# Optimization experiments

Measured on AMD Instinct MI355X. Metric: run time of the kernel, lower is better.

## Reference

```python
import jax, jax.numpy as jnp
import numpy as np

N_NODES = 50000
N_EDGES = 800000
F_IN = 128
F_OUT = 128
N_REL = 4
BN_EPS = 1e-5


def setup_inputs() -> dict:
    key = jax.random.key(0)
    ks = jax.random.split(key, 12)
    s = 1.0 / np.sqrt(F_IN)
    inp = {
        "x": jax.random.normal(ks[0], (N_NODES, F_IN), dtype=jnp.float32),
        "edge_index": jax.random.randint(ks[1], (2, N_EDGES), 0, N_NODES, dtype=jnp.int64),
        "edge_type": jax.random.randint(ks[2], (N_EDGES,), 0, N_REL, dtype=jnp.int64),
        # self-loop linear
        "W_self": jax.random.uniform(ks[3], (F_IN, F_OUT), jnp.float32, -s, s),
        "b_self": jax.random.uniform(ks[4], (F_OUT,), jnp.float32, -s, s),
        # per-relation GIN MLP: Linear -> BatchNorm1d -> ReLU -> Linear (stacked over relations)
        "W1": jax.random.uniform(ks[5], (N_REL, F_IN, F_OUT), jnp.float32, -s, s),
        "b1": jax.random.uniform(ks[6], (N_REL, F_OUT), jnp.float32, -s, s),
        "gamma": jnp.ones((N_REL, F_OUT), jnp.float32),
        "beta": jnp.zeros((N_REL, F_OUT), jnp.float32),
        "W2": jax.random.uniform(ks[7], (N_REL, F_OUT, F_OUT), jnp.float32, -1.0 / np.sqrt(F_OUT), 1.0 / np.sqrt(F_OUT)),
        "b2": jax.random.uniform(ks[8], (N_REL, F_OUT), jnp.float32, -1.0 / np.sqrt(F_OUT), 1.0 / np.sqrt(F_OUT)),
    }
    return inp


def reference(x, edge_index, edge_type, W_self, b_self, W1, b1, gamma, beta, W2, b2):
    N = x.shape[0]
    R = W1.shape[0]
    src, dst = edge_index[0], edge_index[1]
    # single fused scatter-add over (relation, dst): segment id = rel*N + dst
    msg = x[src]                                        # [E, F_in]
    seg = edge_type * N + dst                           # [E]
    agg = jax.ops.segment_sum(msg, seg, num_segments=R * N).reshape(R, N, -1)  # [R, N, F_in]
    # GIN with eps=0: h = x + sum of neighbor messages, per relation
    h = x[None, :, :] + agg                             # [R, N, F_in]
    # MLP: Linear -> BatchNorm1d (batch stats over nodes) -> ReLU -> Linear
    h = jnp.einsum('rnf,rfg->rng', h, W1) + b1[:, None, :]
    mean = jnp.mean(h, axis=1, keepdims=True)
    var = jnp.var(h, axis=1, keepdims=True)
    h = (h - mean) * jax.lax.rsqrt(var + BN_EPS) * gamma[:, None, :] + beta[:, None, :]
    h = jax.nn.relu(h)
    out_rel = jnp.einsum('rng,rgk->rnk', h, W2) + b2[:, None, :]  # [R, N, F_out]
    return x @ W_self + b_self + jnp.sum(out_rel, axis=0)
```

## Files before the change

### kernel.cpp

```cpp
#include <hip/hip_runtime.h>

#define NN 50000
#define NE 800000
#define F 128
#define NREL 4
#define RN (NREL * NN)
#define NB 196
#define BN_EPS 1e-5f
#define TILE 128
#define NT1 391
#define LDW 136
#define CTS 132

typedef __attribute__((ext_vector_type(8))) short short8;
typedef __attribute__((ext_vector_type(4))) float floatx4;

__device__ __forceinline__ ushort f2bf(float f) {
    union { float f; unsigned u; } v; v.f = f;
    unsigned r = v.u + 0x7fffu + ((v.u >> 16) & 1u);
    return (ushort)(r >> 16);
}
__device__ __forceinline__ float bf2f(ushort h) {
    union { unsigned u; float f; } v; v.u = ((unsigned)h) << 16;
    return v.f;
}
__device__ __forceinline__ float ubf(unsigned bits) {
    union { unsigned u; float f; } v; v.u = bits; return v.f;
}
__device__ __forceinline__ unsigned pk2(float a, float b) {
    return (unsigned)f2bf(a) | ((unsigned)f2bf(b) << 16);
}
__device__ __forceinline__ void acc_u4(float* acc, uint4 v) {
    acc[0] += ubf(v.x << 16); acc[1] += ubf(v.x & 0xffff0000u);
    acc[2] += ubf(v.y << 16); acc[3] += ubf(v.y & 0xffff0000u);
    acc[4] += ubf(v.z << 16); acc[5] += ubf(v.z & 0xffff0000u);
    acc[6] += ubf(v.w << 16); acc[7] += ubf(v.w & 0xffff0000u);
}

__global__ __launch_bounds__(256) void xb_kernel(
    const float* __restrict__ x, ushort* __restrict__ xb)
{
    int i = blockIdx.x * 256 + threadIdx.x;
    float4 v = *(const float4*)(x + (size_t)i * 4);
    uint2 u;
    u.x = pk2(v.x, v.y);
    u.y = pk2(v.z, v.w);
    *(uint2*)(xb + (size_t)i * 4) = u;
}

__global__ __launch_bounds__(256) void hist_kernel(
    const int* __restrict__ ei, const int* __restrict__ et, int* __restrict__ counts)
{
    int e = blockIdx.x * 256 + threadIdx.x;
    if (e >= NE) return;
    atomicAdd(&counts[et[e] * NN + ei[NE + e]], 1);
}

__global__ __launch_bounds__(256) void scan1_kernel(
    const int* __restrict__ counts, int* __restrict__ rowptr, int* __restrict__ bsum)
{
    __shared__ int wsum[4];
    const int tid = threadIdx.x;
    const int base = blockIdx.x * 1024 + tid * 4;
    int c[4];
    #pragma unroll
    for (int j = 0; j < 4; j++) c[j] = (base + j < RN) ? counts[base + j] : 0;
    int tsum = c[0] + c[1] + c[2] + c[3];
    const int lane = tid & 63, wv = tid >> 6;
    int s = tsum;
    #pragma unroll
    for (int d = 1; d < 64; d <<= 1) { int t = __shfl_up(s, d); if (lane >= d) s += t; }
    if (lane == 63) wsum[wv] = s;
    __syncthreads();
    int wave_off = 0;
    #pragma unroll
    for (int w = 0; w < 4; w++) if (w < wv) wave_off += wsum[w];
    int run = wave_off + s - tsum;
    #pragma unroll
    for (int j = 0; j < 4; j++) {
        if (base + j < RN) rowptr[base + j] = run;
        run += c[j];
    }
    if (tid == 0) bsum[blockIdx.x] = wsum[0] + wsum[1] + wsum[2] + wsum[3];
}

__global__ __launch_bounds__(256) void scan2_kernel(
    const int* __restrict__ bsum, int* __restrict__ boff, int* __restrict__ rowptr)
{
    __shared__ int wsum[4];
    const int tid = threadIdx.x;
    int v = (tid < NB) ? bsum[tid] : 0;
    const int lane = tid & 63, wv = tid >> 6;
    int s = v;
    #pragma unroll
    for (int d = 1; d < 64; d <<= 1) { int t = __shfl_up(s, d); if (lane >= d) s += t; }
    if (lane == 63) wsum[wv] = s;
    __syncthreads();
    int wave_off = 0;
    #pragma unroll
    for (int w = 0; w < 4; w++) if (w < wv) wave_off += wsum[w];
    if (tid < NB) boff[tid] = wave_off + s - v;
    if (tid == 0) rowptr[RN] = wsum[0] + wsum[1] + wsum[2] + wsum[3];
}

__global__ __launch_bounds__(256) void scan3_kernel(
    int* __restrict__ rowptr, const int* __restrict__ boff, int* __restrict__ cursor)
{
    const int base = blockIdx.x * 1024 + threadIdx.x * 4;
    const int off = boff[blockIdx.x];
    #pragma unroll
    for (int j = 0; j < 4; j++) {
        int idx = base + j;
        if (idx < RN) { int v = rowptr[idx] + off; rowptr[idx] = v; cursor[idx] = v; }
    }
}

__global__ __launch_bounds__(256) void reorder_kernel(
    const int* __restrict__ ei, const int* __restrict__ et,
    int* __restrict__ cursor, int* __restrict__ sorted_src)
{
    int e = blockIdx.x * 256 + threadIdx.x;
    if (e >= NE) return;
    int key = et[e] * NN + ei[NE + e];
    int pos = atomicAdd(&cursor[key], 1);
    sorted_src[pos] = ei[e];
}

__global__ __launch_bounds__(256) void gather_kernel(
    const ushort* __restrict__ xb, const int* __restrict__ rowptr,
    const int* __restrict__ sorted_src, ushort* __restrict__ hbuf)
{
    const int t = blockIdx.x * 256 + threadIdx.x;
    const int row = t >> 4;
    const int lane = t & 15;
    const int n = row % NN;

    const uint4* xv = (const uint4*)xb;
    float acc[8];
    {
        uint4 v = xv[n * 16 + lane];
        acc[0] = ubf(v.x << 16); acc[1] = ubf(v.x & 0xffff0000u);
        acc[2] = ubf(v.y << 16); acc[3] = ubf(v.y & 0xffff0000u);
        acc[4] = ubf(v.z << 16); acc[5] = ubf(v.z & 0xffff0000u);
        acc[6] = ubf(v.w << 16); acc[7] = ubf(v.w & 0xffff0000u);
    }
    int e = rowptr[row];
    const int e1 = rowptr[row + 1];
    for (; e + 4 <= e1; e += 4) {
        int s0 = sorted_src[e], s1 = sorted_src[e + 1];
        int s2 = sorted_src[e + 2], s3 = sorted_src[e + 3];
        uint4 a = xv[s0 * 16 + lane];
        uint4 b = xv[s1 * 16 + lane];
        uint4 c = xv[s2 * 16 + lane];
        uint4 d = xv[s3 * 16 + lane];
        acc_u4(acc, a); acc_u4(acc, b); acc_u4(acc, c); acc_u4(acc, d);
    }
    for (; e < e1; ++e) {
        int s0 = sorted_src[e];
        acc_u4(acc, xv[s0 * 16 + lane]);
    }
    uint4 o;
    o.x = pk2(acc[0], acc[1]);
    o.y = pk2(acc[2], acc[3]);
    o.z = pk2(acc[4], acc[5]);
    o.w = pk2(acc[6], acc[7]);
    *(uint4*)(hbuf + (size_t)row * F + lane * 8) = o;
}

__global__ __launch_bounds__(256) void prep_kernel(
    const float* __restrict__ W1, const float* __restrict__ W2,
    const float* __restrict__ Wself, ushort* __restrict__ Wt_g)
{
    __shared__ ushort Lt[F * F];
    int m = blockIdx.x;
    const float* src = (m < 4) ? (W1 + (size_t)m * F * F)
                     : (m < 8) ? (W2 + (size_t)(m - 4) * F * F)
                               : Wself;
    int tid = threadIdx.x;
    #pragma unroll
    for (int p = 0; p < 16; p++) {
        int i4 = tid + p * 256;
        int k = i4 >> 5;
        int n4 = (i4 & 31) * 4;
        float4 v = *(const float4*)(src + (size_t)k * F + n4);
        Lt[(n4 + 0) * F + k] = f2bf(v.x);
        Lt[(n4 + 1) * F + k] = f2bf(v.y);
        Lt[(n4 + 2) * F + k] = f2bf(v.z);
        Lt[(n4 + 3) * F + k] = f2bf(v.w);
    }
    __syncthreads();
    #pragma unroll
    for (int p = 0; p < 8; p++) {
        int c = tid + p * 256;
        *(uint4*)(Wt_g + (size_t)m * F * F + c * 8) = *(const uint4*)&Lt[c * 8];
    }
}

__global__ __launch_bounds__(256, 4) void gemm1_kernel(
    ushort* __restrict__ hbuf, const ushort* __restrict__ Wt_g,
    const float* __restrict__ b1, float* __restrict__ partials)
{
    __shared__ __attribute__((aligned(16))) ushort Wt[F * LDW];
    __shared__ float csum[F], csq[F];

    const int tid = threadIdx.x;
    const int r = blockIdx.y;
    const int n0 = blockIdx.x * TILE;
    const int lane = tid & 63, w = tid >> 6;
    const int m = lane & 15, quad = lane >> 4;

    if (tid < F) { csum[tid] = 0.f; csq[tid] = 0.f; }

    {
        const ushort* wg = Wt_g + (size_t)r * F * F;
        #pragma unroll
        for (int p = 0; p < 8; p++) {
            int c = tid + p * 256;
            int n = c >> 4, off = (c & 15) * 8;
            *(uint4*)&Wt[n * LDW + off] = *(const uint4*)(wg + c * 8);
        }
    }
    __syncthreads();

    const ushort* Ap0 = hbuf + ((size_t)r * NN + n0 + w * 32 + m) * F + quad * 8;
    const ushort* Ap1 = Ap0 + 16 * F;
    const ushort* Bp  = &Wt[m * LDW + quad * 8];

    floatx4 acc[2][8];
    #pragma unroll
    for (int rg = 0; rg < 2; rg++)
        #pragma unroll
        for (int g = 0; g < 8; g++) acc[rg][g] = (floatx4)0.f;

    #pragma unroll
    for (int kk = 0; kk < 4; kk++) {
        short8 a0 = *(const short8*)(Ap0 + kk * 32);
        short8 a1 = *(const short8*)(Ap1 + kk * 32);
        #pragma unroll
        for (int g = 0; g < 8; g++) {
            short8 b = *(const short8*)(Bp + g * 16 * LDW + kk * 32);
            acc[0][g] = __builtin_amdgcn_mfma_f32_16x16x32_bf16(a0, b, acc[0][g], 0, 0, 0);
            acc[1][g] = __builtin_amdgcn_mfma_f32_16x16x32_bf16(a1, b, acc[1][g], 0, 0, 0);
        }
    }
    __syncthreads();

    ushort* At = Wt;
    #pragma unroll
    for (int rg = 0; rg < 2; rg++) {
        const int rb = w * 32 + rg * 16;
        #pragma unroll
        for (int g = 0; g < 8; g++) {
            int c = g * 16 + m;
            float bv = b1[r * F + c];
            float ls = 0.f, lq = 0.f;
            #pragma unroll
            for (int i = 0; i < 4; i++) {
                int lrow = rb + quad * 4 + i;
                float v = acc[rg][g][i] + bv;
                At[lrow * LDW + c] = f2bf(v);
                if (n0 + lrow < NN) { ls += v; lq += v * v; }
            }
            ls += __shfl_xor(ls, 16); ls += __shfl_xor(ls, 32);
            lq += __shfl_xor(lq, 16); lq += __shfl_xor(lq, 32);
            if (quad == 0) { atomicAdd(&csum[c], ls); atomicAdd(&csq[c], lq); }
        }
    }
    __syncthreads();

    #pragma unroll
    for (int p = 0; p < 8; p++) {
        int cc = tid + p * 256;
        int row = cc >> 4, off = (cc & 15) * 8;
        if (n0 + row < NN)
            *(uint4*)(hbuf + ((size_t)r * NN + n0 + row) * F + off) =
                *(const uint4*)&At[row * LDW + off];
    }
    partials[((size_t)r * NT1 + blockIdx.x) * 256 + tid] =
        (tid < F) ? csum[tid] : csq[tid - F];
}

__global__ __launch_bounds__(256) void bncoef_kernel(
    const float* __restrict__ partials,
    const float* __restrict__ gamma, const float* __restrict__ beta,
    const float* __restrict__ b2, const float* __restrict__ bself,
    float* __restrict__ sa, float* __restrict__ sb, float* __restrict__ btot)
{
    const int tid = threadIdx.x;
    const int pair = blockIdx.x * 8 + (tid >> 5);
    const int l32 = tid & 31;
    const int rel = pair >> 7, col = pair & 127;
    const float* p = partials + (size_t)rel * NT1 * 256;
    float s = 0.f, q = 0.f;
    for (int b = l32; b < NT1; b += 32) {
        s += p[b * 256 + col];
        q += p[b * 256 + 128 + col];
    }
    #pragma unroll
    for (int d = 1; d < 32; d <<= 1) {
        s += __shfl_xor(s, d, 32);
        q += __shfl_xor(q, d, 32);
    }
    if (l32 == 0) {
        float mean = s * (1.0f / NN);
        float var = q * (1.0f / NN) - mean * mean;
        float g = gamma[pair] * rsqrtf(var + BN_EPS);
        sa[pair] = g;
        sb[pair] = beta[pair] - mean * g;
    }
    if (blockIdx.x == 0 && tid < F)
        btot[tid] = bself[tid] + b2[tid] + b2[F + tid] + b2[2 * F + tid] + b2[3 * F + tid];
}

__global__ __launch_bounds__(256, 4) void gemm2_kernel(
    const ushort* __restrict__ xb, const ushort* __restrict__ h1,
    const ushort* __restrict__ Wt_g,
    const float* __restrict__ sa, const float* __restrict__ sb,
    const float* __restrict__ btot, float* __restrict__ out)
{
    __shared__ __attribute__((aligned(16))) ushort Wt[F * LDW];
    __shared__ float sAl[NREL * F], sBl[NREL * F];

    const int tid = threadIdx.x;
    const int n0 = blockIdx.x * TILE;
    const int lane = tid & 63, w = tid >> 6;
    const int m = lane & 15, quad = lane >> 4;
    const int koff = quad * 8;

    #pragma unroll
    for (int p = 0; p < 2; p++) {
        int idx = tid + p * 256;
        sAl[idx] = sa[idx];
        sBl[idx] = sb[idx];
    }

    floatx4 acc[2][8];
    #pragma unroll
    for (int rg = 0; rg < 2; rg++)
        #pragma unroll
        for (int g = 0; g < 8; g++) acc[rg][g] = (floatx4)0.f;

    for (int rel = 0; rel < 5; rel++) {
        __syncthreads();
        {
            int mat = (rel < 4) ? (NREL + rel) : 8;
            const ushort* wg = Wt_g + (size_t)mat * F * F;
            #pragma unroll
            for (int p = 0; p < 8; p++) {
                int c = tid + p * 256;
                int n = c >> 4, off = (c & 15) * 8;
                *(uint4*)&Wt[n * LDW + off] = *(const uint4*)(wg + c * 8);
            }
        }
        __syncthreads();
        const ushort* Bp = &Wt[m * LDW + koff];
        if (rel < 4) {
            const ushort* hp0 = h1 + ((size_t)rel * NN + n0 + w * 32 + m) * F + koff;
            const ushort* hp1 = hp0 + 16 * F;
            #pragma unroll
            for (int kk = 0; kk < 4; kk++) {
                uint4 rv0 = *(const uint4*)(hp0 + kk * 32);
                uint4 rv1 = *(const uint4*)(hp1 + kk * 32);
                float4 ca0 = *(const float4*)(&sAl[rel * F + koff + kk * 32]);
                float4 ca1 = *(const float4*)(&sAl[rel * F + koff + kk * 32 + 4]);
                float4 cb0 = *(const float4*)(&sBl[rel * F + koff + kk * 32]);
                float4 cb1 = *(const float4*)(&sBl[rel * F + koff + kk * 32 + 4]);
                union { uint4 u; short8 s; } a0, a1;
                a0.u.x = pk2(fmaxf(fmaf(ubf(rv0.x << 16),         ca0.x, cb0.x), 0.f),
                             fmaxf(fmaf(ubf(rv0.x & 0xffff0000u), ca0.y, cb0.y), 0.f));
                a0.u.y = pk2(fmaxf(fmaf(ubf(rv0.y << 16),         ca0.z, cb0.z), 0.f),
                             fmaxf(fmaf(ubf(rv0.y & 0xffff0000u), ca0.w, cb0.w), 0.f));
                a0.u.z = pk2(fmaxf(fmaf(ubf(rv0.z << 16),         ca1.x, cb1.x), 0.f),
                             fmaxf(fmaf(ubf(rv0.z & 0xffff0000u), ca1.y, cb1.y), 0.f));
                a0.u.w = pk2(fmaxf(fmaf(ubf(rv0.w << 16),         ca1.z, cb1.z), 0.f),
                             fmaxf(fmaf(ubf(rv0.w & 0xffff0000u), ca1.w, cb1.w), 0.f));
                a1.u.x = pk2(fmaxf(fmaf(ubf(rv1.x << 16),         ca0.x, cb0.x), 0.f),
                             fmaxf(fmaf(ubf(rv1.x & 0xffff0000u), ca0.y, cb0.y), 0.f));
                a1.u.y = pk2(fmaxf(fmaf(ubf(rv1.y << 16),         ca0.z, cb0.z), 0.f),
                             fmaxf(fmaf(ubf(rv1.y & 0xffff0000u), ca0.w, cb0.w), 0.f));
                a1.u.z = pk2(fmaxf(fmaf(ubf(rv1.z << 16),         ca1.x, cb1.x), 0.f),
                             fmaxf(fmaf(ubf(rv1.z & 0xffff0000u), ca1.y, cb1.y), 0.f));
                a1.u.w = pk2(fmaxf(fmaf(ubf(rv1.w << 16),         ca1.z, cb1.z), 0.f),
                             fmaxf(fmaf(ubf(rv1.w & 0xffff0000u), ca1.w, cb1.w), 0.f));
                #pragma unroll
                for (int g = 0; g < 8; g++) {
                    short8 b = *(const short8*)(Bp + g * 16 * LDW + kk * 32);
                    acc[0][g] = __builtin_amdgcn_mfma_f32_16x16x32_bf16(a0.s, b, acc[0][g], 0, 0, 0);
                    acc[1][g] = __builtin_amdgcn_mfma_f32_16x16x32_bf16(a1.s, b, acc[1][g], 0, 0, 0);
                }
            }
        } else {
            const ushort* xp0 = xb + (size_t)(n0 + w * 32 + m) * F + koff;
            const ushort* xp1 = xp0 + 16 * F;
            #pragma unroll
            for (int kk = 0; kk < 4; kk++) {
                short8 a0 = *(const short8*)(xp0 + kk * 32);
                short8 a1 = *(const short8*)(xp1 + kk * 32);
                #pragma unroll
                for (int g = 0; g < 8; g++) {
                    short8 b = *(const short8*)(Bp + g * 16 * LDW + kk * 32);
                    acc[0][g] = __builtin_amdgcn_mfma_f32_16x16x32_bf16(a0, b, acc[0][g], 0, 0, 0);
                    acc[1][g] = __builtin_amdgcn_mfma_f32_16x16x32_bf16(a1, b, acc[1][g], 0, 0, 0);
                }
            }
        }
    }

    float* Ct = (float*)Wt;
    #pragma unroll
    for (int half = 0; half < 2; half++) {
        __syncthreads();
        if ((w >> 1) == half) {
            const int wl = w & 1;
            #pragma unroll
            for (int rg = 0; rg < 2; rg++) {
                const int rb = wl * 32 + rg * 16;
                #pragma unroll
                for (int g = 0; g < 8; g++) {
                    int c = g * 16 + m;
                    float bv = btot[c];
                    #pragma unroll
                    for (int i = 0; i < 4; i++) {
                        int lrow = rb + quad * 4 + i;
                        Ct[lrow * CTS + c] = acc[rg][g][i] + bv;
                    }
                }
            }
        }
        __syncthreads();
        #pragma unroll
        for (int p = 0; p < 8; p++) {
            int i4 = tid + p * 256;
            int row = i4 >> 5;
            int c4 = (i4 & 31) * 4;
            int n = n0 + half * 64 + row;
            if (n < NN)
                *(float4*)(out + (size_t)n * F + c4) = *(const float4*)&Ct[row * CTS + c4];
        }
    }
}

extern "C" void kernel_launch(void* const* d_in, const int* in_sizes, int n_in,
                              void* d_out, int out_size, void* d_ws, size_t ws_size,
                              hipStream_t stream) {
    const float* x     = (const float*)d_in[0];
    const int*   ei    = (const int*)d_in[1];
    const int*   et    = (const int*)d_in[2];
    const float* Wself = (const float*)d_in[3];
    const float* bself = (const float*)d_in[4];
    const float* W1    = (const float*)d_in[5];
    const float* b1    = (const float*)d_in[6];
    const float* gamma = (const float*)d_in[7];
    const float* beta  = (const float*)d_in[8];
    const float* W2    = (const float*)d_in[9];
    const float* b2    = (const float*)d_in[10];
    float* out = (float*)d_out;

    ushort* hbuf = (ushort*)d_ws;
    ushort* xb   = hbuf + (size_t)RN * F;
    ushort* Wt_g = xb + (size_t)NN * F;
    float*  partials = (float*)(Wt_g + 9 * F * F);
    float*  sa    = partials + (size_t)NREL * NT1 * 256;
    float*  sb    = sa + NREL * F;
    float*  btot  = sb + NREL * F;
    int* counts     = (int*)(btot + F);
    int* rowptr     = counts + RN;
    int* cursor     = rowptr + RN + 1;
    int* sorted_src = cursor + RN;
    int* bsum       = sorted_src + NE;
    int* boff       = bsum + 256;

    hipMemsetAsync(counts, 0, (size_t)RN * sizeof(int), stream);

    prep_kernel<<<9, 256, 0, stream>>>(W1, W2, Wself, Wt_g);
    xb_kernel<<<NN * F / 1024, 256, 0, stream>>>(x, xb);
    hist_kernel<<<(NE + 255) / 256, 256, 0, stream>>>(ei, et, counts);
    scan1_kernel<<<NB, 256, 0, stream>>>(counts, rowptr, bsum);
    scan2_kernel<<<1, 256, 0, stream>>>(bsum, boff, rowptr);
    scan3_kernel<<<NB, 256, 0, stream>>>(rowptr, boff, cursor);
    reorder_kernel<<<(NE + 255) / 256, 256, 0, stream>>>(ei, et, cursor, sorted_src);
    gather_kernel<<<RN * 16 / 256, 256, 0, stream>>>(xb, rowptr, sorted_src, hbuf);
    {
        dim3 grid(NT1, NREL);
        gemm1_kernel<<<grid, 256, 0, stream>>>(hbuf, Wt_g, b1, partials);
    }
    bncoef_kernel<<<64, 256, 0, stream>>>(partials, gamma, beta, b2, bself, sa, sb, btot);
    gemm2_kernel<<<NT1, 256, 0, stream>>>(xb, hbuf, Wt_g, sa, sb, btot, out);
}
```

Baseline: 344.9 us.

## Merge prep kernels, fold scan2 into scan3, widen gemm2 to 512 threads

Merges the bf16 conversion of x, the weight transpose and the edge histogram into one launch. It also folds the single-block block-sum scan into scan3, where every block rescans the 196 partial sums itself. Together these remove three kernel launches and their dependency gaps. gemm2 now uses 512 threads with 16 rows per wave, so each wave holds half the accumulators, in exchange for less A-operand reuse per wave. The merged prep kernel reserves 32KB of LDS for every block, which may lower occupancy for the xb and histogram blocks.

```diff
diff --git a/kernel.cpp b/kernel.cpp
--- a/kernel.cpp
+++ b/kernel.cpp
@@ -11,6 +11,8 @@
 #define NT1 391
 #define LDW 136
 #define CTS 132
+#define XBB 6250
+#define HISTB 3125
 
 typedef __attribute__((ext_vector_type(8))) short short8;
 typedef __attribute__((ext_vector_type(4))) float floatx4;
@@ -19,10 +21,6 @@
     union { float f; unsigned u; } v; v.f = f;
     unsigned r = v.u + 0x7fffu + ((v.u >> 16) & 1u);
     return (ushort)(r >> 16);
-}
-__device__ __forceinline__ float bf2f(ushort h) {
-    union { unsigned u; float f; } v; v.u = ((unsigned)h) << 16;
-    return v.f;
 }
 __device__ __forceinline__ float ubf(unsigned bits) {
     union { unsigned u; float f; } v; v.u = bits; return v.f;
@@ -37,23 +35,48 @@
     acc[6] += ubf(v.w << 16); acc[7] += ubf(v.w & 0xffff0000u);
 }
 
-__global__ __launch_bounds__(256) void xb_kernel(
-    const float* __restrict__ x, ushort* __restrict__ xb)
-{
-    int i = blockIdx.x * 256 + threadIdx.x;
-    float4 v = *(const float4*)(x + (size_t)i * 4);
-    uint2 u;
-    u.x = pk2(v.x, v.y);
-    u.y = pk2(v.z, v.w);
-    *(uint2*)(xb + (size_t)i * 4) = u;
-}
-
-__global__ __launch_bounds__(256) void hist_kernel(
+__global__ __launch_bounds__(256) void prep_all_kernel(
+    const float* __restrict__ x, ushort* __restrict__ xb,
+    const float* __restrict__ W1, const float* __restrict__ W2,
+    const float* __restrict__ Wself, ushort* __restrict__ Wt_g,
     const int* __restrict__ ei, const int* __restrict__ et, int* __restrict__ counts)
 {
-    int e = blockIdx.x * 256 + threadIdx.x;
-    if (e >= NE) return;
-    atomicAdd(&counts[et[e] * NN + ei[NE + e]], 1);
+    __shared__ ushort Lt[F * F];
+    const int tid = threadIdx.x;
+    const int b = blockIdx.x;
+    if (b < XBB) {
+        int i = b * 256 + tid;
+        float4 v = *(const float4*)(x + (size_t)i * 4);
+        uint2 u;
+        u.x = pk2(v.x, v.y);
+        u.y = pk2(v.z, v.w);
+        *(uint2*)(xb + (size_t)i * 4) = u;
+    } else if (b < XBB + 9) {
+        int m = b - XBB;
+        const float* src = (m < 4) ? (W1 + (size_t)m * F * F)
+                         : (m < 8) ? (W2 + (size_t)(m - 4) * F * F)
+                                   : Wself;
+        #pragma unroll
+        for (int p = 0; p < 16; p++) {
+            int i4 = tid + p * 256;
+            int k = i4 >> 5;
+            int n4 = (i4 & 31) * 4;
+            float4 v = *(const float4*)(src + (size_t)k * F + n4);
+            Lt[(n4 + 0) * F + k] = f2bf(v.x);
+            Lt[(n4 + 1) * F + k] = f2bf(v.y);
+            Lt[(n4 + 2) * F + k] = f2bf(v.z);
+            Lt[(n4 + 3) * F + k] = f2bf(v.w);
+        }
+        __syncthreads();
+        #pragma unroll
+        for (int p = 0; p < 8; p++) {
+            int c = tid + p * 256;
+            *(uint4*)(Wt_g + (size_t)m * F * F + c * 8) = *(const uint4*)&Lt[c * 8];
+        }
+    } else {
+        int e = (b - XBB - 9) * 256 + tid;
+        if (e < NE) atomicAdd(&counts[et[e] * NN + ei[NE + e]], 1);
+    }
 }
 
 __global__ __launch_bounds__(256) void scan1_kernel(
@@ -84,10 +107,11 @@
     if (tid == 0) bsum[blockIdx.x] = wsum[0] + wsum[1] + wsum[2] + wsum[3];
 }
 
-__global__ __launch_bounds__(256) void scan2_kernel(
-    const int* __restrict__ bsum, int* __restrict__ boff, int* __restrict__ rowptr)
+__global__ __launch_bounds__(256) void scan3_kernel(
+    int* __restrict__ rowptr, const int* __restrict__ bsum, int* __restrict__ cursor)
 {
     __shared__ int wsum[4];
+    __shared__ int sx[256];
     const int tid = threadIdx.x;
     int v = (tid < NB) ? bsum[tid] : 0;
     const int lane = tid & 63, wv = tid >> 6;
@@ -99,19 +123,16 @@
     int wave_off = 0;
     #pragma unroll
     for (int w = 0; w < 4; w++) if (w < wv) wave_off += wsum[w];
-    if (tid < NB) boff[tid] = wave_off + s - v;
-    if (tid == 0) rowptr[RN] = wsum[0] + wsum[1] + wsum[2] + wsum[3];
-}
-
-__global__ __launch_bounds__(256) void scan3_kernel(
-    int* __restrict__ rowptr, const int* __restrict__ boff, int* __restrict__ cursor)
-{
-    const int base = blockIdx.x * 1024 + threadIdx.x * 4;
-    const int off = boff[blockIdx.x];
+    sx[tid] = wave_off + s - v;
+    __syncthreads();
+    const int off = sx[blockIdx.x];
+    if (blockIdx.x == 0 && tid == 0)
+        rowptr[RN] = wsum[0] + wsum[1] + wsum[2] + wsum[3];
+    const int base = blockIdx.x * 1024 + tid * 4;
     #pragma unroll
     for (int j = 0; j < 4; j++) {
         int idx = base + j;
-        if (idx < RN) { int v = rowptr[idx] + off; rowptr[idx] = v; cursor[idx] = v; }
+        if (idx < RN) { int t = rowptr[idx] + off; rowptr[idx] = t; cursor[idx] = t; }
     }
 }
 
@@ -165,35 +186,6 @@
     o.z = pk2(acc[4], acc[5]);
     o.w = pk2(acc[6], acc[7]);
     *(uint4*)(hbuf + (size_t)row * F + lane * 8) = o;
-}
-
-__global__ __launch_bounds__(256) void prep_kernel(
-    const float* __restrict__ W1, const float* __restrict__ W2,
-    const float* __restrict__ Wself, ushort* __restrict__ Wt_g)
-{
-    __shared__ ushort Lt[F * F];
-    int m = blockIdx.x;
-    const float* src = (m < 4) ? (W1 + (size_t)m * F * F)
-                     : (m < 8) ? (W2 + (size_t)(m - 4) * F * F)
-                               : Wself;
-    int tid = threadIdx.x;
-    #pragma unroll
-    for (int p = 0; p < 16; p++) {
-        int i4 = tid + p * 256;
-        int k = i4 >> 5;
-        int n4 = (i4 & 31) * 4;
-        float4 v = *(const float4*)(src + (size_t)k * F + n4);
-        Lt[(n4 + 0) * F + k] = f2bf(v.x);
-        Lt[(n4 + 1) * F + k] = f2bf(v.y);
-        Lt[(n4 + 2) * F + k] = f2bf(v.z);
-        Lt[(n4 + 3) * F + k] = f2bf(v.w);
-    }
-    __syncthreads();
-    #pragma unroll
-    for (int p = 0; p < 8; p++) {
-        int c = tid + p * 256;
-        *(uint4*)(Wt_g + (size_t)m * F * F + c * 8) = *(const uint4*)&Lt[c * 8];
-    }
 }
 
 __global__ __launch_bounds__(256, 4) void gemm1_kernel(
@@ -289,7 +281,8 @@
     const int tid = threadIdx.x;
     const int pair = blockIdx.x * 8 + (tid >> 5);
     const int l32 = tid & 31;
-    const int rel = pair >> 7, col = pair & 127;
+    const int rel = pair >> 7;
+    const int col = pair & 127;
     const float* p = partials + (size_t)rel * NT1 * 256;
     float s = 0.f, q = 0.f;
     for (int b = l32; b < NT1; b += 32) {
@@ -312,7 +305,7 @@
         btot[tid] = bself[tid] + b2[tid] + b2[F + tid] + b2[2 * F + tid] + b2[3 * F + tid];
 }
 
-__global__ __launch_bounds__(256, 4) void gemm2_kernel(
+__global__ __launch_bounds__(512, 2) void gemm2_kernel(
     const ushort* __restrict__ xb, const ushort* __restrict__ h1,
     const ushort* __restrict__ Wt_g,
     const float* __restrict__ sa, const float* __restrict__ sb,
@@ -327,18 +320,12 @@
     const int m = lane & 15, quad = lane >> 4;
     const int koff = quad * 8;
 
-    #pragma unroll
-    for (int p = 0; p < 2; p++) {
-        int idx = tid + p * 256;
-        sAl[idx] = sa[idx];
-        sBl[idx] = sb[idx];
-    }
-
-    floatx4 acc[2][8];
-    #pragma unroll
-    for (int rg = 0; rg < 2; rg++)
-        #pragma unroll
-        for (int g = 0; g < 8; g++) acc[rg][g] = (floatx4)0.f;
+    sAl[tid] = sa[tid];
+    sBl[tid] = sb[tid];
+
+    floatx4 acc[8];
+    #pragma unroll
+    for (int g = 0; g < 8; g++) acc[g] = (floatx4)0.f;
 
     for (int rel = 0; rel < 5; rel++) {
         __syncthreads();
@@ -346,8 +333,8 @@
             int mat = (rel < 4) ? (NREL + rel) : 8;
             const ushort* wg = Wt_g + (size_t)mat * F * F;
             #pragma unroll
-            for (int p = 0; p < 8; p++) {
-                int c = tid + p * 256;
+            for (int p = 0; p < 4; p++) {
+                int c = tid + p * 512;
                 int n = c >> 4, off = (c & 15) * 8;
                 *(uint4*)&Wt[n * LDW + off] = *(const uint4*)(wg + c * 8);
             }
@@ -355,52 +342,38 @@
         __syncthreads();
         const ushort* Bp = &Wt[m * LDW + koff];
         if (rel < 4) {
-            const ushort* hp0 = h1 + ((size_t)rel * NN + n0 + w * 32 + m) * F + koff;
-            const ushort* hp1 = hp0 + 16 * F;
+            const ushort* hp = h1 + ((size_t)rel * NN + n0 + w * 16 + m) * F + koff;
             #pragma unroll
             for (int kk = 0; kk < 4; kk++) {
-                uint4 rv0 = *(const uint4*)(hp0 + kk * 32);
-                uint4 rv1 = *(const uint4*)(hp1 + kk * 32);
+                uint4 rv = *(const uint4*)(hp + kk * 32);
                 float4 ca0 = *(const float4*)(&sAl[rel * F + koff + kk * 32]);
                 float4 ca1 = *(const float4*)(&sAl[rel * F + koff + kk * 32 + 4]);
                 float4 cb0 = *(const float4*)(&sBl[rel * F + koff + kk * 32]);
                 float4 cb1 = *(const float4*)(&sBl[rel * F + koff + kk * 32 + 4]);
-                union { uint4 u; short8 s; } a0, a1;
-                a0.u.x = pk2(fmaxf(fmaf(ubf(rv0.x << 16),         ca0.x, cb0.x), 0.f),
-                             fmaxf(fmaf(ubf(rv0.x & 0xffff0000u), ca0.y, cb0.y), 0.f));
-                a0.u.y = pk2(fmaxf(fmaf(ubf(rv0.y << 16),         ca0.z, cb0.z), 0.f),
-                             fmaxf(fmaf(ubf(rv0.y & 0xffff0000u), ca0.w, cb0.w), 0.f));
-                a0.u.z = pk2(fmaxf(fmaf(ubf(rv0.z << 16),         ca1.x, cb1.x), 0.f),
-                             fmaxf(fmaf(ubf(rv0.z & 0xffff0000u), ca1.y, cb1.y), 0.f));
-                a0.u.w = pk2(fmaxf(fmaf(ubf(rv0.w << 16),         ca1.z, cb1.z), 0.f),
-                             fmaxf(fmaf(ubf(rv0.w & 0xffff0000u), ca1.w, cb1.w), 0.f));
-                a1.u.x = pk2(fmaxf(fmaf(ubf(rv1.x << 16),         ca0.x, cb0.x), 0.f),
-                             fmaxf(fmaf(ubf(rv1.x & 0xffff0000u), ca0.y, cb0.y), 0.f));
-                a1.u.y = pk2(fmaxf(fmaf(ubf(rv1.y << 16),         ca0.z, cb0.z), 0.f),
-                             fmaxf(fmaf(ubf(rv1.y & 0xffff0000u), ca0.w, cb0.w), 0.f));
-                a1.u.z = pk2(fmaxf(fmaf(ubf(rv1.z << 16),         ca1.x, cb1.x), 0.f),
-                             fmaxf(fmaf(ubf(rv1.z & 0xffff0000u), ca1.y, cb1.y), 0.f));
-                a1.u.w = pk2(fmaxf(fmaf(ubf(rv1.w << 16),         ca1.z, cb1.z), 0.f),
-                             fmaxf(fmaf(ubf(rv1.w & 0xffff0000u), ca1.w, cb1.w), 0.f));
+                union { uint4 u; short8 s; } a0;
+                a0.u.x = pk2(fmaxf(fmaf(ubf(rv.x << 16),         ca0.x, cb0.x), 0.f),
+                             fmaxf(fmaf(ubf(rv.x & 0xffff0000u), ca0.y, cb0.y), 0.f));
+                a0.u.y = pk2(fmaxf(fmaf(ubf(rv.y << 16),         ca0.z, cb0.z), 0.f),
+                             fmaxf(fmaf(ubf(rv.y & 0xffff0000u), ca0.w, cb0.w), 0.f));
+                a0.u.z = pk2(fmaxf(fmaf(ubf(rv.z << 16),         ca1.x, cb1.x), 0.f),
+                             fmaxf(fmaf(ubf(rv.z & 0xffff0000u), ca1.y, cb1.y), 0.f));
+                a0.u.w = pk2(fmaxf(fmaf(ubf(rv.w << 16),         ca1.z, cb1.z), 0.f),
+                             fmaxf(fmaf(ubf(rv.w & 0xffff0000u), ca1.w, cb1.w), 0.f));
                 #pragma unroll
                 for (int g = 0; g < 8; g++) {
                     short8 b = *(const short8*)(Bp + g * 16 * LDW + kk * 32);
-                    acc[0][g] = __builtin_amdgcn_mfma_f32_16x16x32_bf16(a0.s, b, acc[0][g], 0, 0, 0);
-                    acc[1][g] = __builtin_amdgcn_mfma_f32_16x16x32_bf16(a1.s, b, acc[1][g], 0, 0, 0);
+                    acc[g] = __builtin_amdgcn_mfma_f32_16x16x32_bf16(a0.s, b, acc[g], 0, 0, 0);
                 }
             }
         } else {
-            const ushort* xp0 = xb + (size_t)(n0 + w * 32 + m) * F + koff;
-            const ushort* xp1 = xp0 + 16 * F;
+            const ushort* xp = xb + (size_t)(n0 + w * 16 + m) * F + koff;
             #pragma unroll
             for (int kk = 0; kk < 4; kk++) {
-                short8 a0 = *(const short8*)(xp0 + kk * 32);
-                short8 a1 = *(const short8*)(xp1 + kk * 32);
+                short8 a0 = *(const short8*)(xp + kk * 32);
                 #pragma unroll
                 for (int g = 0; g < 8; g++) {
                     short8 b = *(const short8*)(Bp + g * 16 * LDW + kk * 32);
-                    acc[0][g] = __builtin_amdgcn_mfma_f32_16x16x32_bf16(a0, b, acc[0][g], 0, 0, 0);
-                    acc[1][g] = __builtin_amdgcn_mfma_f32_16x16x32_bf16(a1, b, acc[1][g], 0, 0, 0);
+                    acc[g] = __builtin_amdgcn_mfma_f32_16x16x32_bf16(a0, b, acc[g], 0, 0, 0);
                 }
             }
         }
@@ -410,27 +383,23 @@
     #pragma unroll
     for (int half = 0; half < 2; half++) {
         __syncthreads();
-        if ((w >> 1) == half) {
-            const int wl = w & 1;
+        if ((w >> 2) == half) {
+            const int rb = (w & 3) * 16;
             #pragma unroll
-            for (int rg = 0; rg < 2; rg++) {
-                const int rb = wl * 32 + rg * 16;
+            for (int g = 0; g < 8; g++) {
+                int c = g * 16 + m;
+                float bv = btot[c];
                 #pragma unroll
-                for (int g = 0; g < 8; g++) {
-                    int c = g * 16 + m;
-                    float bv = btot[c];
-                    #pragma unroll
-                    for (int i = 0; i < 4; i++) {
-                        int lrow = rb + quad * 4 + i;
-                        Ct[lrow * CTS + c] = acc[rg][g][i] + bv;
-                    }
+                for (int i = 0; i < 4; i++) {
+                    int lrow = rb + quad * 4 + i;
+                    Ct[lrow * CTS + c] = acc[g][i] + bv;
                 }
             }
         }
         __syncthreads();
         #pragma unroll
-        for (int p = 0; p < 8; p++) {
-            int i4 = tid + p * 256;
+        for (int p = 0; p < 4; p++) {
+            int i4 = tid + p * 512;
             int row = i4 >> 5;
             int c4 = (i4 & 31) * 4;
             int n = n0 + half * 64 + row;
@@ -468,16 +437,13 @@
     int* cursor     = rowptr + RN + 1;
     int* sorted_src = cursor + RN;
     int* bsum       = sorted_src + NE;
-    int* boff       = bsum + 256;
 
     hipMemsetAsync(counts, 0, (size_t)RN * sizeof(int), stream);
 
-    prep_kernel<<<9, 256, 0, stream>>>(W1, W2, Wself, Wt_g);
-    xb_kernel<<<NN * F / 1024, 256, 0, stream>>>(x, xb);
-    hist_kernel<<<(NE + 255) / 256, 256, 0, stream>>>(ei, et, counts);
+    prep_all_kernel<<<XBB + 9 + HISTB, 256, 0, stream>>>(
+        x, xb, W1, W2, Wself, Wt_g, ei, et, counts);
     scan1_kernel<<<NB, 256, 0, stream>>>(counts, rowptr, bsum);
-    scan2_kernel<<<1, 256, 0, stream>>>(bsum, boff, rowptr);
-    scan3_kernel<<<NB, 256, 0, stream>>>(rowptr, boff, cursor);
+    scan3_kernel<<<NB, 256, 0, stream>>>(rowptr, bsum, cursor);
     reorder_kernel<<<(NE + 255) / 256, 256, 0, stream>>>(ei, et, cursor, sorted_src);
     gather_kernel<<<RN * 16 / 256, 256, 0, stream>>>(xb, rowptr, sorted_src, hbuf);
     {
@@ -485,5 +451,5 @@
         gemm1_kernel<<<grid, 256, 0, stream>>>(hbuf, Wt_g, b1, partials);
     }
     bncoef_kernel<<<64, 256, 0, stream>>>(partials, gamma, beta, b2, bself, sa, sb, btot);
-    gemm2_kernel<<<NT1, 256, 0, stream>>>(xb, hbuf, Wt_g, sa, sb, btot, out);
-}
+    gemm2_kernel<<<NT1, 512, 0, stream>>>(xb, hbuf, Wt_g, sa, sb, btot, out);
+}
```

New measurement: 288.3 us. 1.2x faster.
